# Kernel optimization log

Measured on AMD Instinct MI355X. Metric: run time of the kernel, lower is better.

Reference implementation:

```python
import jax, jax.numpy as jnp
import numpy as np

TAU = 1.0  # gumbel_temperature
K = 8      # number of template rows (hard-coded for SCAN)


def _forward(decodings, type_emb, w_sem, b_sem, gumbel, target_types, spans):
    B, N, M, V = decodings.shape
    # --- per-example template logits: decoder_sem[span-2][type-9](type_embedding[type]) ---
    emb = type_emb[target_types]                  # [B,H]
    w = w_sem[target_types - 9]                   # [B, K*(N+1), H]
    b = b_sem[target_types - 9]                   # [B, K*(N+1)]
    logits = (jnp.einsum('bkh,bh->bk', w, emb) + b).reshape(B, K, N + 1)
    # ragged span: only positions 0..span are valid (original views to (K, s+1))
    pos = jnp.arange(N + 1)
    valid_pos = pos[None, None, :] <= spans[:, None, None]
    logits = jnp.where(valid_pos, logits, jnp.float32(-1e30))
    logp = jax.nn.log_softmax(logits, axis=-1)
    # hard gumbel-softmax with straight-through estimator (F.gumbel_softmax hard=True)
    y_soft = jax.nn.softmax((logp + gumbel) / TAU, axis=-1)
    y_hard = jax.nn.one_hot(jnp.argmax(y_soft, -1), N + 1, dtype=y_soft.dtype)
    dt = y_hard + y_soft - jax.lax.stop_gradient(y_soft)     # [B,K,N+1]
    # special start template for target type 20: row 0 selects child 1, rest select pad (0)
    start = jax.nn.one_hot(jnp.where(jnp.arange(K) == 0, 1, 0), N + 1, dtype=dt.dtype)
    dt = jnp.where((target_types == 20)[:, None, None], start[None], dt)
    # --- apply_decoder_template ---
    pad = jnp.zeros((M, V), decodings.dtype).at[:, 0].set(1.0)  # pad vector, token 0
    choices = jnp.concatenate(
        [jnp.broadcast_to(pad[None, None], (B, 1, M, V)), decodings], axis=1)  # [B,N+1,M,V]
    out = jnp.einsum('bkn,bnmv->bkmv', dt, choices)              # [B,K,M,V]
    # per-template effective length: last position whose argmax token != 0
    out_idx = jnp.argmax(out, axis=-1)                           # [B,K,M]
    jpos = jnp.arange(M)
    lens = jnp.max(jnp.where(out_idx != 0, jpos + 1, 0), axis=-1).astype(jnp.int32)  # [B,K]
    # sequential packing of the K template outputs, clipped at M (scan over K=8)
    def step(idx, l):
        eff = jnp.minimum(l, M - idx)
        return idx + eff, (idx, eff)
    _, (offsets, effs) = jax.lax.scan(step, jnp.zeros(B, jnp.int32), lens.T)
    offsets, effs = offsets.T, effs.T                            # [B,K]
    dest = offsets[:, :, None] + jpos[None, None, :]             # [B,K,M]
    valid = jpos[None, None, :] < effs[:, :, None]
    dest = jnp.where(valid, dest, M)                             # dump invalid writes to row M
    bidx = jnp.arange(B)[:, None, None]
    vals = jnp.where(valid[..., None], out, 0.0)
    result = jnp.zeros((B, M + 1, V), decodings.dtype)
    result = result.at[bidx, dest].set(vals)
    return result[:, :M]                                         # new_d: [B,M,V]


def setup_inputs() -> dict:
    key = jax.random.key(0)
    ks = jax.random.split(key, 6)
    B, N, M, V, H, T = 256, 16, 128, 64, 128, 24
    decodings = jax.random.normal(ks[0], (B, N, M, V), jnp.float32)
    type_emb = jax.random.normal(ks[1], (T, H), jnp.float32)
    w_sem = jax.random.normal(ks[2], (T - 9, K * (N + 1), H), jnp.float32) * 0.05
    b_sem = jnp.zeros((T - 9, K * (N + 1)), jnp.float32)
    u = jax.random.uniform(ks[3], (B, K, N + 1), jnp.float32, 1e-6, 1.0 - 1e-6)
    gumbel = -jnp.log(-jnp.log(u))
    target_types = jax.random.randint(ks[4], (B,), 9, T)  # valid decoder_sem type range
    spans = jnp.full((B,), N, dtype=jnp.int32)
    return {"decodings": decodings, "type_emb": type_emb, "w_sem": w_sem,
            "b_sem": b_sem, "gumbel": gumbel, "target_types": target_types,
            "spans": spans}


def reference(decodings, type_emb, w_sem, b_sem, gumbel, target_types, spans):
    return _forward(decodings, type_emb, w_sem, b_sem, gumbel, target_types, spans)
```

## Files before the change

kernel.cpp:

```cpp
#include <hip/hip_runtime.h>

constexpr int Bn  = 256;
constexpr int Nn  = 16;
constexpr int Mn  = 128;
constexpr int Vn  = 64;
constexpr int Hn  = 128;
constexpr int Kn  = 8;
constexpr int NP1 = 17;
constexpr int KN  = Kn * NP1;

__global__ __launch_bounds__(512) void fused_template_pack(
    const float* __restrict__ dec,
    const float* __restrict__ type_emb,
    const float* __restrict__ w_sem,
    const float* __restrict__ b_sem,
    const float* __restrict__ gumbel,
    const int*   __restrict__ ttypes,
    const int*   __restrict__ spans,
    float*       __restrict__ out)
{
    const int b    = blockIdx.x;
    const int tid  = threadIdx.x;
    const int lane = tid & 63;
    const int wave = tid >> 6;

    __shared__ float s_scores[KN];
    __shared__ int   s_sel[Kn];
    __shared__ int   s_len[Kn];
    __shared__ int   s_off[Kn];
    __shared__ int   s_eff[Kn];
    __shared__ int   s_total;

    const int t    = ttypes[b];
    const int span = spans[b];

    if (t != 20) {
        if (tid < KN) {
            const int n = tid % NP1;
            float score = -1e30f;
            if (n <= span) {
                const float4* wrow = (const float4*)(w_sem + ((size_t)(t - 9) * KN + tid) * Hn);
                const float4* erow = (const float4*)(type_emb + (size_t)t * Hn);
                float acc = 0.f;
                #pragma unroll
                for (int i = 0; i < Hn / 4; ++i) {
                    float4 wv = wrow[i];
                    float4 ev = erow[i];
                    acc += wv.x * ev.x + wv.y * ev.y + wv.z * ev.z + wv.w * ev.w;
                }
                score = acc + b_sem[(t - 9) * KN + tid] + gumbel[(size_t)b * KN + tid];
            }
            s_scores[tid] = score;
        }
        __syncthreads();
        if (tid < Kn) {
            int best = 0;
            float bv = s_scores[tid * NP1];
            #pragma unroll
            for (int n = 1; n < NP1; ++n) {
                float v = s_scores[tid * NP1 + n];
                if (v > bv) { bv = v; best = n; }
            }
            s_sel[tid] = best;
        }
    } else {
        if (tid < Kn) s_sel[tid] = (tid == 0) ? 1 : 0;
    }
    __syncthreads();

    if (wave < Kn) {
        const int s = s_sel[wave];
        int len = 0;
        if (s > 0) {
            const float* row = dec + (((size_t)b * Nn + (s - 1)) * Mn) * Vn;
            for (int m = Mn - 1; m >= 0; --m) {
                float bv = row[(size_t)m * Vn + lane];
                int   bi = lane;
                #pragma unroll
                for (int d = 1; d < 64; d <<= 1) {
                    float ov = __shfl_xor(bv, d, 64);
                    int   oi = __shfl_xor(bi, d, 64);
                    if (ov > bv || (ov == bv && oi < bi)) { bv = ov; bi = oi; }
                }
                if (bi != 0) { len = m + 1; break; }
            }
        }
        if (lane == 0) s_len[wave] = len;
    }
    __syncthreads();

    if (tid == 0) {
        int idx = 0;
        #pragma unroll
        for (int k = 0; k < Kn; ++k) {
            const int eff = min(s_len[k], Mn - idx);
            s_off[k] = idx;
            s_eff[k] = eff;
            idx += eff;
        }
        s_total = idx;
    }
    __syncthreads();

    float4* outb = (float4*)(out + (size_t)b * Mn * Vn);
    for (int k = 0; k < Kn; ++k) {
        const int eff = s_eff[k];
        if (eff == 0) continue;
        const float4* src =
            (const float4*)(dec + (((size_t)b * Nn + (s_sel[k] - 1)) * Mn) * Vn);
        float4* dst = outb + (size_t)s_off[k] * (Vn / 4);
        const int cnt = eff * (Vn / 4);
        for (int i = tid; i < cnt; i += 512) dst[i] = src[i];
    }

    const int total = s_total;
    const int zcnt  = (Mn - total) * (Vn / 4);
    float4* zdst = outb + (size_t)total * (Vn / 4);
    const float4 zero = make_float4(0.f, 0.f, 0.f, 0.f);
    for (int i = tid; i < zcnt; i += 512) zdst[i] = zero;
}

extern "C" void kernel_launch(void* const* d_in, const int* in_sizes, int n_in,
                              void* d_out, int out_size, void* d_ws, size_t ws_size,
                              hipStream_t stream) {
    const float* dec      = (const float*)d_in[0];
    const float* type_emb = (const float*)d_in[1];
    const float* w_sem    = (const float*)d_in[2];
    const float* b_sem    = (const float*)d_in[3];
    const float* gumbel   = (const float*)d_in[4];
    const int*   ttypes   = (const int*)d_in[5];
    const int*   spans    = (const int*)d_in[6];
    float* out = (float*)d_out;

    fused_template_pack<<<Bn, 512, 0, stream>>>(
        dec, type_emb, w_sem, b_sem, gumbel, ttypes, spans, out);
}
```

Baseline: 181.1 us.

## Compute lengths for all children speculatively, overlapping template scoring

Waves 0-3 now compute the effective length of all 16 child decodings at once. They batch-load the last four rows of each child before running the argmax reductions. The template-logit dot products run at the same time on the last 136 threads, so the dependent chain of score, select, then length scan is gone. Every thread recomputes the packing offsets in registers, which removes two block barriers and one serial shared-memory step. The cost is redundant length scans for children that may not be selected.

```diff
diff --git a/kernel.cpp b/kernel.cpp
--- a/kernel.cpp
+++ b/kernel.cpp
@@ -8,6 +8,18 @@
 constexpr int Kn  = 8;
 constexpr int NP1 = 17;
 constexpr int KN  = Kn * NP1;
+
+__device__ __forceinline__ bool wave_argmax_is_nonzero(float v, int lane) {
+    float bv = v;
+    int   bi = lane;
+    #pragma unroll
+    for (int d = 1; d < 64; d <<= 1) {
+        float ov = __shfl_xor(bv, d, 64);
+        int   oi = __shfl_xor(bi, d, 64);
+        if (ov > bv || (ov == bv && oi < bi)) { bv = ov; bi = oi; }
+    }
+    return bi != 0;
+}
 
 __global__ __launch_bounds__(512) void fused_template_pack(
     const float* __restrict__ dec,
@@ -25,35 +37,67 @@
     const int wave = tid >> 6;
 
     __shared__ float s_scores[KN];
+    __shared__ int   s_clen[Nn];
     __shared__ int   s_sel[Kn];
     __shared__ int   s_len[Kn];
-    __shared__ int   s_off[Kn];
-    __shared__ int   s_eff[Kn];
-    __shared__ int   s_total;
 
     const int t    = ttypes[b];
     const int span = spans[b];
 
-    if (t != 20) {
-        if (tid < KN) {
-            const int n = tid % NP1;
-            float score = -1e30f;
-            if (n <= span) {
-                const float4* wrow = (const float4*)(w_sem + ((size_t)(t - 9) * KN + tid) * Hn);
-                const float4* erow = (const float4*)(type_emb + (size_t)t * Hn);
-                float acc = 0.f;
-                #pragma unroll
-                for (int i = 0; i < Hn / 4; ++i) {
-                    float4 wv = wrow[i];
-                    float4 ev = erow[i];
-                    acc += wv.x * ev.x + wv.y * ev.y + wv.z * ev.z + wv.w * ev.w;
+    if (wave < 4) {
+        const float* base = dec + (size_t)b * Nn * Mn * Vn + lane;
+        float g[4][4];
+        #pragma unroll
+        for (int j = 0; j < 4; ++j) {
+            const float* row = base + (size_t)(wave * 4 + j) * Mn * Vn;
+            #pragma unroll
+            for (int p = 0; p < 4; ++p)
+                g[j][p] = row[(size_t)(127 - p) * Vn];
+        }
+        #pragma unroll
+        for (int j = 0; j < 4; ++j) {
+            int len = 0;
+            #pragma unroll
+            for (int p = 0; p < 4; ++p) {
+                if (len == 0 && wave_argmax_is_nonzero(g[j][p], lane))
+                    len = 128 - p;
+            }
+            if (len == 0) {
+                const float* row = base + (size_t)(wave * 4 + j) * Mn * Vn;
+                for (int m = Mn - 5; m >= 0; --m) {
+                    if (wave_argmax_is_nonzero(row[(size_t)m * Vn], lane)) {
+                        len = m + 1;
+                        break;
+                    }
                 }
-                score = acc + b_sem[(t - 9) * KN + tid] + gumbel[(size_t)b * KN + tid];
             }
-            s_scores[tid] = score;
+            if (lane == 0) s_clen[wave * 4 + j] = len;
         }
-        __syncthreads();
-        if (tid < Kn) {
+    }
+
+    if (t != 20 && tid >= 512 - KN) {
+        const int j = tid - (512 - KN);
+        const int n = j % NP1;
+        float score = -1e30f;
+        if (n <= span) {
+            const float4* wrow = (const float4*)(w_sem + ((size_t)(t - 9) * KN + j) * Hn);
+            const float4* erow = (const float4*)(type_emb + (size_t)t * Hn);
+            float acc = 0.f;
+            #pragma unroll
+            for (int i = 0; i < Hn / 4; ++i) {
+                float4 wv = wrow[i];
+                float4 ev = erow[i];
+                acc += wv.x * ev.x + wv.y * ev.y + wv.z * ev.z + wv.w * ev.w;
+            }
+            score = acc + b_sem[(t - 9) * KN + j] + gumbel[(size_t)b * KN + j];
+        }
+        s_scores[j] = score;
+    }
+    __syncthreads();
+
+    if (tid < Kn) {
+        int sel;
+        if (t != 20) {
             int best = 0;
             float bv = s_scores[tid * NP1];
             #pragma unroll
@@ -61,61 +105,39 @@
                 float v = s_scores[tid * NP1 + n];
                 if (v > bv) { bv = v; best = n; }
             }
-            s_sel[tid] = best;
+            sel = best;
+        } else {
+            sel = (tid == 0) ? 1 : 0;
         }
-    } else {
-        if (tid < Kn) s_sel[tid] = (tid == 0) ? 1 : 0;
+        s_sel[tid] = sel;
+        s_len[tid] = (sel > 0) ? s_clen[sel - 1] : 0;
     }
     __syncthreads();
 
-    if (wave < Kn) {
-        const int s = s_sel[wave];
-        int len = 0;
-        if (s > 0) {
-            const float* row = dec + (((size_t)b * Nn + (s - 1)) * Mn) * Vn;
-            for (int m = Mn - 1; m >= 0; --m) {
-                float bv = row[(size_t)m * Vn + lane];
-                int   bi = lane;
-                #pragma unroll
-                for (int d = 1; d < 64; d <<= 1) {
-                    float ov = __shfl_xor(bv, d, 64);
-                    int   oi = __shfl_xor(bi, d, 64);
-                    if (ov > bv || (ov == bv && oi < bi)) { bv = ov; bi = oi; }
-                }
-                if (bi != 0) { len = m + 1; break; }
-            }
-        }
-        if (lane == 0) s_len[wave] = len;
+    int off[Kn], eff[Kn], sel_r[Kn];
+    int idx = 0;
+    #pragma unroll
+    for (int k = 0; k < Kn; ++k) {
+        sel_r[k] = s_sel[k];
+        const int e = min(s_len[k], Mn - idx);
+        off[k] = idx;
+        eff[k] = e;
+        idx += e;
     }
-    __syncthreads();
-
-    if (tid == 0) {
-        int idx = 0;
-        #pragma unroll
-        for (int k = 0; k < Kn; ++k) {
-            const int eff = min(s_len[k], Mn - idx);
-            s_off[k] = idx;
-            s_eff[k] = eff;
-            idx += eff;
-        }
-        s_total = idx;
-    }
-    __syncthreads();
 
     float4* outb = (float4*)(out + (size_t)b * Mn * Vn);
+    #pragma unroll
     for (int k = 0; k < Kn; ++k) {
-        const int eff = s_eff[k];
-        if (eff == 0) continue;
+        if (eff[k] == 0) continue;
         const float4* src =
-            (const float4*)(dec + (((size_t)b * Nn + (s_sel[k] - 1)) * Mn) * Vn);
-        float4* dst = outb + (size_t)s_off[k] * (Vn / 4);
-        const int cnt = eff * (Vn / 4);
+            (const float4*)(dec + (((size_t)b * Nn + (sel_r[k] - 1)) * Mn) * Vn);
+        float4* dst = outb + (size_t)off[k] * (Vn / 4);
+        const int cnt = eff[k] * (Vn / 4);
         for (int i = tid; i < cnt; i += 512) dst[i] = src[i];
     }
 
-    const int total = s_total;
-    const int zcnt  = (Mn - total) * (Vn / 4);
-    float4* zdst = outb + (size_t)total * (Vn / 4);
+    const int zcnt = (Mn - idx) * (Vn / 4);
+    float4* zdst = outb + (size_t)idx * (Vn / 4);
     const float4 zero = make_float4(0.f, 0.f, 0.f, 0.f);
     for (int i = tid; i < zcnt; i += 512) zdst[i] = zero;
 }
```

After: 179.2 us. No clear change (-1.0%).
